# Kernel optimization log

Hardware: AMD Instinct MI355X
Metric: run time of the kernel (lower is better)

## Reference

```python
import jax, jax.numpy as jnp
import numpy as np

DIM = 1024
HEADS = 16
DIM_HEAD = 64
CHUNK = 64
INNER = HEADS * DIM_HEAD  # 1024


def setup_inputs() -> dict:
    key = jax.random.key(0)
    k1, k2, k3 = jax.random.split(key, 3)
    x = jax.random.normal(k1, (4, 4096, DIM), dtype=jnp.float32)
    # nn.Linear weights stored as (out, in); apply as x @ W.T
    w_qkv = jax.random.normal(k2, (INNER * 3, DIM), dtype=jnp.float32) * (DIM ** -0.5)
    w_out = jax.random.normal(k3, (DIM, INNER), dtype=jnp.float32) * (INNER ** -0.5)
    b_out = jnp.zeros((DIM,), dtype=jnp.float32)
    return {"x": x, "w_qkv": w_qkv, "w_out": w_out, "b_out": b_out}


def reference(x, w_qkv, w_out, b_out):
    b, n, _ = x.shape
    scale = DIM_HEAD ** -0.5
    qkv = jnp.einsum('bnd,ed->bne', x, w_qkv)  # (b, n, 3*inner)
    q, k, v = jnp.split(qkv, 3, axis=-1)
    nblk = n // CHUNK

    def to_blocks(t):
        # (b, n, h*d) -> (b, h, nblk, c, d)
        t = t.reshape(b, n, HEADS, DIM_HEAD).transpose(0, 2, 1, 3)
        return t.reshape(b, HEADS, nblk, CHUNK, DIM_HEAD)

    qb, kb, vb = to_blocks(q), to_blocks(k), to_blocks(v)
    scores = jnp.einsum('bhgqd,bhgkd->bhgqk', qb, kb) * scale  # block-local
    attn = jax.nn.softmax(scores, axis=-1)
    ob = jnp.einsum('bhgqk,bhgkd->bhgqd', attn, vb)
    out = ob.reshape(b, HEADS, n, DIM_HEAD).transpose(0, 2, 1, 3).reshape(b, n, INNER)
    return jnp.einsum('bne,de->bnd', out, w_out) + b_out
```

## Files before the change

### kernel.cpp

```cpp
#include <hip/hip_runtime.h>
#include <stdint.h>

typedef __attribute__((ext_vector_type(8))) short bf16x8;
typedef __attribute__((ext_vector_type(4))) float f32x4;

__device__ __forceinline__ unsigned short bf16_of(float f) {
  union { float f; uint32_t u; } x; x.f = f;
  uint32_t r = x.u + 0x7fffu + ((x.u >> 16) & 1u);
  return (unsigned short)(r >> 16);
}

#define GLD16(gp, lp) __builtin_amdgcn_global_load_lds( \
    (const __attribute__((address_space(1))) uint32_t*)(gp), \
    (__attribute__((address_space(3))) uint32_t*)(lp), 16, 0, 0)

#define BAR() do { asm volatile("" ::: "memory"); __builtin_amdgcn_s_barrier(); asm volatile("" ::: "memory"); } while (0)

__global__ void cvt_all(const float* __restrict__ x, const float* __restrict__ wq,
                        const float* __restrict__ wo,
                        unsigned short* __restrict__ xb, unsigned short* __restrict__ wqb,
                        unsigned short* __restrict__ wob) {
  const int N_X = 4194304, N_WQ = 786432, N_WO = 262144;
  const int total = N_X + N_WQ + N_WO;
  int i = blockIdx.x * blockDim.x + threadIdx.x;
  int stride = gridDim.x * blockDim.x;
  for (int j = i; j < total; j += stride) {
    const float* src; unsigned short* dst; int off;
    if (j < N_X)            { src = x;  dst = xb;  off = j; }
    else if (j < N_X + N_WQ){ src = wq; dst = wqb; off = j - N_X; }
    else                    { src = wo; dst = wob; off = j - N_X - N_WQ; }
    float4 f = ((const float4*)src)[off];
    union { unsigned short s[4]; uint2 v; } u;
    u.s[0] = bf16_of(f.x); u.s[1] = bf16_of(f.y);
    u.s[2] = bf16_of(f.z); u.s[3] = bf16_of(f.w);
    ((uint2*)dst)[off] = u.v;
  }
}

template<int BIAS, int OUTF32, int GW, int NSEG>
__global__ __launch_bounds__(512, 2)
void gemm256h(const unsigned short* __restrict__ A,
              const unsigned short* __restrict__ B,
              void* __restrict__ C, const float* __restrict__ bias,
              int N, int K)
{
  __shared__ __align__(1024) unsigned short sm[65536];
  char* const smb = (char*)sm;
  const int tid = threadIdx.x, w = tid >> 6, lane = tid & 63;
  const int wm = w >> 2, wn = w & 3;
  const int fr = lane & 15, kg = lane >> 4;
  const int swz = (fr & 7) << 4;
  const int srow = lane >> 3, sslot = lane & 7;
  const int cXcd = blockIdx.x & 7, iIdx = blockIdx.x >> 3;
  const int NT_tot = NSEG * 16;

  auto tileMN = [&](int s, int& mt, int& nt) {
    const int T = cXcd * (32 * NSEG) + s * 32 + iIdx;
    const int g = T / (64 * GW), rr = T % (64 * GW);
    mt = rr / GW; nt = g * GW + rr % GW;
  };

  int stOff[2][2];
  #pragma unroll
  for (int h = 0; h < 2; ++h)
    #pragma unroll
    for (int i2 = 0; i2 < 2; ++i2)
      stOff[h][i2] = (h * 128 + (i2 * 8 + w) * 8 + srow) * K + (sslot ^ srow) * 8;

  int curMt, curNt, nxtMt, nxtNt;
  tileMN(0, curMt, curNt);
  nxtMt = curMt; nxtNt = curNt;
  if (NSEG > 1) tileMN(1, nxtMt, nxtNt);
  const unsigned short* aSeg  = A + ((size_t)curMt << 8) * K;
  const unsigned short* bSeg  = B + ((size_t)curNt << 8) * K;
  const unsigned short* aSegN = A + ((size_t)nxtMt << 8) * K;
  const unsigned short* bSegN = B + ((size_t)nxtNt << 8) * K;

  auto STAGEh = [&](const unsigned short* src, int opnd, int half, int parity) {
    char* region = smb + opnd * 65536 + parity * 32768 + half * 16384;
    GLD16(src + stOff[half][0], region + w * 1024);
    GLD16(src + stOff[half][1], region + (8 + w) * 1024);
  };
  auto LDA = [&](char* Ab, int j, int kk) -> bf16x8 {
    const int r = 32 * j + 16 * wm + fr;
    return *(const bf16x8*)(Ab + r * 128 + ((kk * 64 + kg * 16) ^ swz));
  };
  auto LDB = [&](char* Bb, int l, int kk) -> bf16x8 {
    const int r = 64 * l + 16 * wn + fr;
    return *(const bf16x8*)(Bb + r * 128 + ((kk * 64 + kg * 16) ^ swz));
  };

  f32x4 acc[8][4] = {};

  STAGEh(bSeg, 1, 0, 0);
  STAGEh(aSeg, 0, 0, 0);
  STAGEh(bSeg, 1, 1, 0);
  STAGEh(aSeg, 0, 1, 0);

  for (int s = 0; s < NSEG; ++s) {
    for (int tt = 0; tt < 16; ++tt) {
      const int T = s * 16 + tt;
      char* Ab = smb + (T & 1) * 32768;
      char* Bb = smb + 65536 + (T & 1) * 32768;

      asm volatile("s_waitcnt vmcnt(0)" ::: "memory");
      BAR();

      bf16x8 a[4][2], bb[4][2];
      #pragma unroll
      for (int l = 0; l < 4; ++l) { bb[l][0] = LDB(Bb, l, 0); bb[l][1] = LDB(Bb, l, 1); }
      #pragma unroll
      for (int j = 0; j < 4; ++j) { a[j][0] = LDA(Ab, j, 0); a[j][1] = LDA(Ab, j, 1); }

      if (T + 1 < NT_tot) {
        const int p1 = (T + 1) & 1;
        const unsigned short *aS, *bS;
        if (tt < 15) { aS = aSeg + ((tt + 1) << 6); bS = bSeg + ((tt + 1) << 6); }
        else         { aS = aSegN;                  bS = bSegN; }
        STAGEh(bS, 1, 0, p1);
        STAGEh(aS, 0, 0, p1);
        STAGEh(bS, 1, 1, p1);
        STAGEh(aS, 0, 1, p1);
      }

      __builtin_amdgcn_s_setprio(1);
      #pragma unroll
      for (int kk = 0; kk < 2; ++kk)
        #pragma unroll
        for (int j = 0; j < 4; ++j)
          #pragma unroll
          for (int l = 0; l < 4; ++l)
            acc[j][l] = __builtin_amdgcn_mfma_f32_16x16x32_bf16(a[j][kk], bb[l][kk], acc[j][l], 0, 0, 0);
      __builtin_amdgcn_s_setprio(0);

      #pragma unroll
      for (int j = 0; j < 4; ++j) { a[j][0] = LDA(Ab, j + 4, 0); a[j][1] = LDA(Ab, j + 4, 1); }
      __builtin_amdgcn_s_setprio(1);
      #pragma unroll
      for (int kk = 0; kk < 2; ++kk)
        #pragma unroll
        for (int j = 0; j < 4; ++j)
          #pragma unroll
          for (int l = 0; l < 4; ++l)
            acc[j + 4][l] = __builtin_amdgcn_mfma_f32_16x16x32_bf16(a[j][kk], bb[l][kk], acc[j + 4][l], 0, 0, 0);
      __builtin_amdgcn_s_setprio(0);
    }

    const int bm0 = curMt << 8, bn0 = curNt << 8;
    #pragma unroll
    for (int l = 0; l < 4; ++l) {
      const int col = bn0 + 64 * l + 16 * wn + fr;
      float bb2 = 0.0f;
      if (BIAS && OUTF32) bb2 = bias[col];
      #pragma unroll
      for (int j = 0; j < 8; ++j) {
        const int row0 = bm0 + 32 * j + 16 * wm + kg * 4;
        #pragma unroll
        for (int rr = 0; rr < 4; ++rr) {
          if (OUTF32)
            ((float*)C)[(size_t)(row0 + rr) * N + col] = acc[j][l][rr] + bb2;
          else
            ((unsigned short*)C)[(size_t)(row0 + rr) * N + col] = bf16_of(acc[j][l][rr]);
        }
      }
    }
    #pragma unroll
    for (int j = 0; j < 8; ++j)
      #pragma unroll
      for (int l = 0; l < 4; ++l)
        acc[j][l] = f32x4{0.f, 0.f, 0.f, 0.f};

    curMt = nxtMt; curNt = nxtNt;
    aSeg = aSegN; bSeg = bSegN;
    if (s + 2 < NSEG) {
      tileMN(s + 2, nxtMt, nxtNt);
      aSegN = A + ((size_t)nxtMt << 8) * K;
      bSegN = B + ((size_t)nxtNt << 8) * K;
    }
  }
}

__global__ __launch_bounds__(256, 4)
void attn_block(const unsigned short* __restrict__ qkv,
                unsigned short* __restrict__ o)
{
  __shared__ __align__(1024) unsigned short Qs[64 * 64];
  __shared__ __align__(1024) unsigned short Ks[64 * 64];
  __shared__ __align__(1024) unsigned short Vt[64 * 64];
  __shared__ __align__(1024) unsigned short Ps[64 * 64];
  __shared__ __align__(1024) unsigned short Os[64 * 64];
  const int tid = threadIdx.x, w = tid >> 6, lane = tid & 63;
  const int g = blockIdx.x, h = blockIdx.y, b = blockIdx.z;
  const size_t mbase = (size_t)b * 4096 + (size_t)g * 64;
  const unsigned short* qg = qkv + mbase * 3072 + h * 64;
  const unsigned short* kgl = qkv + mbase * 3072 + 1024 + h * 64;
  const unsigned short* vg = qkv + mbase * 3072 + 2048 + h * 64;

  #pragma unroll
  for (int i = 0; i < 2; ++i) {
    const int chunk = i * 4 + w;
    const int row = chunk * 8 + (lane >> 3);
    const int c8 = (lane & 7) ^ (row & 7);
    GLD16(qg + (size_t)row * 3072 + c8 * 8, (char*)Qs + chunk * 1024);
    GLD16(kgl + (size_t)row * 3072 + c8 * 8, (char*)Ks + chunk * 1024);
  }
  #pragma unroll
  for (int i = 0; i < 2; ++i) {
    const int c = i * 256 + tid;
    const int n = c >> 3, d0 = (c & 7) * 8;
    bf16x8 v = *(const bf16x8*)(vg + (size_t)n * 3072 + d0);
    #pragma unroll
    for (int j = 0; j < 8; ++j) {
      const int d = d0 + j;
      const int bo = d * 128 + n * 2;
      *(unsigned short*)((char*)Vt + (bo ^ ((d & 7) << 4))) = (unsigned short)v[j];
    }
  }
  __syncthreads();

  const int fr = lane & 15, kg = lane >> 4;
  f32x4 s[4] = {};
  #pragma unroll
  for (int kt = 0; kt < 2; ++kt) {
    const int kb = kt * 64 + kg * 16;
    const int rq = w * 16 + fr;
    bf16x8 aq = *(const bf16x8*)((const char*)Qs + rq * 128 + (kb ^ ((rq & 7) << 4)));
    #pragma unroll
    for (int nf = 0; nf < 4; ++nf) {
      const int rk = nf * 16 + fr;
      bf16x8 bk = *(const bf16x8*)((const char*)Ks + rk * 128 + (kb ^ ((rk & 7) << 4)));
      s[nf] = __builtin_amdgcn_mfma_f32_16x16x32_bf16(aq, bk, s[nf], 0, 0, 0);
    }
  }

  const float scale = 0.125f;
  float inv[4];
  #pragma unroll
  for (int r = 0; r < 4; ++r) {
    float m0 = fmaxf(fmaxf(s[0][r], s[1][r]), fmaxf(s[2][r], s[3][r]));
    #pragma unroll
    for (int d = 1; d < 16; d <<= 1) m0 = fmaxf(m0, __shfl_xor(m0, d));
    float sum = 0.0f;
    #pragma unroll
    for (int nf = 0; nf < 4; ++nf) {
      float p = __expf((s[nf][r] - m0) * scale);
      s[nf][r] = p;
      sum += p;
    }
    #pragma unroll
    for (int d = 1; d < 16; d <<= 1) sum += __shfl_xor(sum, d);
    inv[r] = 1.0f / sum;
  }

  #pragma unroll
  for (int r = 0; r < 4; ++r) {
    const int m = w * 16 + kg * 4 + r;
    #pragma unroll
    for (int nf = 0; nf < 4; ++nf) {
      const int bo = m * 128 + (nf * 16 + fr) * 2;
      *(unsigned short*)((char*)Ps + (bo ^ ((m & 7) << 4))) = bf16_of(s[nf][r] * inv[r]);
    }
  }
  __syncthreads();

  f32x4 oa[4] = {};
  #pragma unroll
  for (int kt = 0; kt < 2; ++kt) {
    const int kb = kt * 64 + kg * 16;
    const int rp = w * 16 + fr;
    bf16x8 ap = *(const bf16x8*)((const char*)Ps + rp * 128 + (kb ^ ((rp & 7) << 4)));
    #pragma unroll
    for (int df = 0; df < 4; ++df) {
      const int rv = df * 16 + fr;
      bf16x8 bv = *(const bf16x8*)((const char*)Vt + rv * 128 + (kb ^ ((rv & 7) << 4)));
      oa[df] = __builtin_amdgcn_mfma_f32_16x16x32_bf16(ap, bv, oa[df], 0, 0, 0);
    }
  }

  #pragma unroll
  for (int df = 0; df < 4; ++df) {
    #pragma unroll
    for (int r = 0; r < 4; ++r) {
      const int m = w * 16 + kg * 4 + r;
      const int bo = m * 128 + (df * 16 + fr) * 2;
      *(unsigned short*)((char*)Os + (bo ^ ((m & 7) << 4))) = bf16_of(oa[df][r]);
    }
  }
  __syncthreads();
  {
    const int row = tid >> 2;
    const int sb = (tid & 3) * 32;
    const int sw = (row & 7) << 4;
    char* rp = (char*)Os + row * 128;
    uint4 v0 = *(uint4*)(rp + (sb ^ sw));
    uint4 v1 = *(uint4*)(rp + ((sb + 16) ^ sw));
    char* op = (char*)(o + (mbase + row) * 1024 + h * 64) + sb;
    *(uint4*)op = v0;
    *(uint4*)(op + 16) = v1;
  }
}

extern "C" void kernel_launch(void* const* d_in, const int* in_sizes, int n_in,
                              void* d_out, int out_size, void* d_ws, size_t ws_size,
                              hipStream_t stream) {
  const float* x     = (const float*)d_in[0];
  const float* w_qkv = (const float*)d_in[1];
  const float* w_out = (const float*)d_in[2];
  const float* b_out = (const float*)d_in[3];
  char* ws = (char*)d_ws;
  const size_t SZ_X  = (size_t)16384 * 1024 * 2;
  const size_t SZ_WQ = (size_t)3072 * 1024 * 2;
  const size_t SZ_WO = (size_t)1024 * 1024 * 2;
  unsigned short* xb  = (unsigned short*)ws;
  unsigned short* wqb = (unsigned short*)(ws + SZ_X);
  unsigned short* wob = (unsigned short*)(ws + SZ_X + SZ_WQ);
  unsigned short* qkv = (unsigned short*)(ws + SZ_X + SZ_WQ + SZ_WO);
  unsigned short* ob  = xb;

  cvt_all<<<2048, 256, 0, stream>>>(x, w_qkv, w_out, xb, wqb, wob);
  gemm256h<0,0,6,3><<<dim3(256), 512, 0, stream>>>(xb, wqb, qkv, nullptr, 3072, 1024);
  attn_block<<<dim3(64, 16, 4), 256, 0, stream>>>(qkv, ob);
  gemm256h<1,1,4,1><<<dim3(256), 512, 0, stream>>>(ob, wob, d_out, b_out, 1024, 1024);
}
```

Measured before the change: 173.5 us.

## Fuse block-local attention with output projection in one kernel

Replaces the separate attention kernel and the output-projection GEMM with one kernel. Each 512-thread workgroup owns 64 rows and loops over all 16 heads: four waves compute attention for the current head, then all eight waves multiply the result by the matching slice of w_out, accumulating into registers. The next head's Q/K/V are double-buffered so their loads overlap the current head's work. This removes the intermediate attention-output round trip through global memory and one launch. In exchange, only 256 single-workgroup blocks run, half the waves sit idle during the attention phase, and w_out is read straight from global memory with no LDS reuse.

```diff
diff --git a/kernel.cpp b/kernel.cpp
--- a/kernel.cpp
+++ b/kernel.cpp
@@ -180,123 +180,163 @@
   }
 }
 
-__global__ __launch_bounds__(256, 4)
-void attn_block(const unsigned short* __restrict__ qkv,
-                unsigned short* __restrict__ o)
+__global__ __launch_bounds__(512, 1)
+void attn_out(const unsigned short* __restrict__ qkv,
+              const unsigned short* __restrict__ wo,
+              const float* __restrict__ bias,
+              float* __restrict__ out)
 {
-  __shared__ __align__(1024) unsigned short Qs[64 * 64];
-  __shared__ __align__(1024) unsigned short Ks[64 * 64];
-  __shared__ __align__(1024) unsigned short Vt[64 * 64];
-  __shared__ __align__(1024) unsigned short Ps[64 * 64];
-  __shared__ __align__(1024) unsigned short Os[64 * 64];
+  __shared__ __align__(1024) unsigned short Qs[2][64 * 64];
+  __shared__ __align__(1024) unsigned short Ks[2][64 * 64];
+  __shared__ __align__(1024) unsigned short Vt[2][64 * 64];
+  __shared__ __align__(1024) unsigned short Pb[64 * 64];
+  __shared__ __align__(1024) unsigned short oaB[64 * 64];
   const int tid = threadIdx.x, w = tid >> 6, lane = tid & 63;
-  const int g = blockIdx.x, h = blockIdx.y, b = blockIdx.z;
-  const size_t mbase = (size_t)b * 4096 + (size_t)g * 64;
-  const unsigned short* qg = qkv + mbase * 3072 + h * 64;
-  const unsigned short* kgl = qkv + mbase * 3072 + 1024 + h * 64;
-  const unsigned short* vg = qkv + mbase * 3072 + 2048 + h * 64;
+  const int fr = lane & 15, kg = lane >> 4;
+  const size_t mb = (size_t)blockIdx.x * 64;
+  const unsigned short* base = qkv + mb * 3072;
+
+  const int srow = w * 8 + (lane >> 3);
+  const int sslot = (lane & 7) ^ (srow & 7);
+  const int vn = tid >> 3, vd0 = (tid & 7) * 8;
+  const float scale = 0.125f;
+
+  f32x4 acc[4][8] = {};
+  bf16x8 vreg;
+
+  GLD16(base + (size_t)srow * 3072 + sslot * 8, (char*)Qs[0] + w * 1024);
+  GLD16(base + (size_t)srow * 3072 + 1024 + sslot * 8, (char*)Ks[0] + w * 1024);
+  vreg = *(const bf16x8*)(base + (size_t)vn * 3072 + 2048 + vd0);
+
+  for (int h = 0; h < 16; ++h) {
+    const int p = h & 1;
+
+    asm volatile("s_waitcnt vmcnt(0)" ::: "memory");
+    #pragma unroll
+    for (int j = 0; j < 8; ++j) {
+      const int d = vd0 + j;
+      const int bo = d * 128 + vn * 2;
+      *(unsigned short*)((char*)Vt[p] + (bo ^ ((d & 7) << 4))) = (unsigned short)vreg[j];
+    }
+    asm volatile("s_waitcnt lgkmcnt(0)" ::: "memory");
+    BAR();
+
+    if (h < 15) {
+      const int q = p ^ 1;
+      const unsigned short* nb = base + (h + 1) * 64;
+      GLD16(nb + (size_t)srow * 3072 + sslot * 8, (char*)Qs[q] + w * 1024);
+      GLD16(nb + (size_t)srow * 3072 + 1024 + sslot * 8, (char*)Ks[q] + w * 1024);
+      vreg = *(const bf16x8*)(nb + (size_t)vn * 3072 + 2048 + vd0);
+    }
+
+    if (w < 4) {
+      f32x4 s[4] = {};
+      #pragma unroll
+      for (int kt = 0; kt < 2; ++kt) {
+        const int kb = kt * 64 + kg * 16;
+        const int rq = w * 16 + fr;
+        bf16x8 aq = *(const bf16x8*)((const char*)Qs[p] + rq * 128 + (kb ^ ((rq & 7) << 4)));
+        #pragma unroll
+        for (int nf = 0; nf < 4; ++nf) {
+          const int rk = nf * 16 + fr;
+          bf16x8 bk = *(const bf16x8*)((const char*)Ks[p] + rk * 128 + (kb ^ ((rk & 7) << 4)));
+          s[nf] = __builtin_amdgcn_mfma_f32_16x16x32_bf16(aq, bk, s[nf], 0, 0, 0);
+        }
+      }
+      float inv[4];
+      #pragma unroll
+      for (int r = 0; r < 4; ++r) {
+        float m0 = fmaxf(fmaxf(s[0][r], s[1][r]), fmaxf(s[2][r], s[3][r]));
+        #pragma unroll
+        for (int d = 1; d < 16; d <<= 1) m0 = fmaxf(m0, __shfl_xor(m0, d));
+        float sum = 0.0f;
+        #pragma unroll
+        for (int nf = 0; nf < 4; ++nf) {
+          float pv = __expf((s[nf][r] - m0) * scale);
+          s[nf][r] = pv;
+          sum += pv;
+        }
+        #pragma unroll
+        for (int d = 1; d < 16; d <<= 1) sum += __shfl_xor(sum, d);
+        inv[r] = 1.0f / sum;
+      }
+      #pragma unroll
+      for (int r = 0; r < 4; ++r) {
+        const int m = w * 16 + kg * 4 + r;
+        #pragma unroll
+        for (int nf = 0; nf < 4; ++nf) {
+          const int bo = m * 128 + (nf * 16 + fr) * 2;
+          *(unsigned short*)((char*)Pb + (bo ^ ((m & 7) << 4))) = bf16_of(s[nf][r] * inv[r]);
+        }
+      }
+      f32x4 oa[4] = {};
+      #pragma unroll
+      for (int kt = 0; kt < 2; ++kt) {
+        const int kb = kt * 64 + kg * 16;
+        const int rp = w * 16 + fr;
+        bf16x8 ap = *(const bf16x8*)((const char*)Pb + rp * 128 + (kb ^ ((rp & 7) << 4)));
+        #pragma unroll
+        for (int df = 0; df < 4; ++df) {
+          const int rv = df * 16 + fr;
+          bf16x8 bv = *(const bf16x8*)((const char*)Vt[p] + rv * 128 + (kb ^ ((rv & 7) << 4)));
+          oa[df] = __builtin_amdgcn_mfma_f32_16x16x32_bf16(ap, bv, oa[df], 0, 0, 0);
+        }
+      }
+      #pragma unroll
+      for (int df = 0; df < 4; ++df) {
+        #pragma unroll
+        for (int r = 0; r < 4; ++r) {
+          const int m = w * 16 + kg * 4 + r;
+          const int bo = m * 128 + (df * 16 + fr) * 2;
+          *(unsigned short*)((char*)oaB + (bo ^ ((m & 7) << 4))) = bf16_of(oa[df][r]);
+        }
+      }
+    }
+
+    bf16x8 bf[8][2];
+    {
+      const unsigned short* ws0 = wo + 64 * h + kg * 8;
+      #pragma unroll
+      for (int nf = 0; nf < 8; ++nf) {
+        const size_t d = (size_t)(128 * w + 16 * nf + fr);
+        bf[nf][0] = *(const bf16x8*)(ws0 + d * 1024);
+        bf[nf][1] = *(const bf16x8*)(ws0 + d * 1024 + 32);
+      }
+    }
+
+    BAR();
+    asm volatile("s_waitcnt vmcnt(0)" ::: "memory");
+
+    bf16x8 afr[4][2];
+    #pragma unroll
+    for (int jm = 0; jm < 4; ++jm) {
+      const int r = 16 * jm + fr;
+      afr[jm][0] = *(const bf16x8*)((const char*)oaB + r * 128 + ((kg * 16) ^ ((r & 7) << 4)));
+      afr[jm][1] = *(const bf16x8*)((const char*)oaB + r * 128 + ((64 + kg * 16) ^ ((r & 7) << 4)));
+    }
+    __builtin_amdgcn_s_setprio(1);
+    #pragma unroll
+    for (int kk = 0; kk < 2; ++kk)
+      #pragma unroll
+      for (int jm = 0; jm < 4; ++jm)
+        #pragma unroll
+        for (int nf = 0; nf < 8; ++nf)
+          acc[jm][nf] = __builtin_amdgcn_mfma_f32_16x16x32_bf16(afr[jm][kk], bf[nf][kk], acc[jm][nf], 0, 0, 0);
+    __builtin_amdgcn_s_setprio(0);
+    BAR();
+  }
 
   #pragma unroll
-  for (int i = 0; i < 2; ++i) {
-    const int chunk = i * 4 + w;
-    const int row = chunk * 8 + (lane >> 3);
-    const int c8 = (lane & 7) ^ (row & 7);
-    GLD16(qg + (size_t)row * 3072 + c8 * 8, (char*)Qs + chunk * 1024);
-    GLD16(kgl + (size_t)row * 3072 + c8 * 8, (char*)Ks + chunk * 1024);
-  }
-  #pragma unroll
-  for (int i = 0; i < 2; ++i) {
-    const int c = i * 256 + tid;
-    const int n = c >> 3, d0 = (c & 7) * 8;
-    bf16x8 v = *(const bf16x8*)(vg + (size_t)n * 3072 + d0);
-    #pragma unroll
-    for (int j = 0; j < 8; ++j) {
-      const int d = d0 + j;
-      const int bo = d * 128 + n * 2;
-      *(unsigned short*)((char*)Vt + (bo ^ ((d & 7) << 4))) = (unsigned short)v[j];
-    }
-  }
-  __syncthreads();
-
-  const int fr = lane & 15, kg = lane >> 4;
-  f32x4 s[4] = {};
-  #pragma unroll
-  for (int kt = 0; kt < 2; ++kt) {
-    const int kb = kt * 64 + kg * 16;
-    const int rq = w * 16 + fr;
-    bf16x8 aq = *(const bf16x8*)((const char*)Qs + rq * 128 + (kb ^ ((rq & 7) << 4)));
-    #pragma unroll
-    for (int nf = 0; nf < 4; ++nf) {
-      const int rk = nf * 16 + fr;
-      bf16x8 bk = *(const bf16x8*)((const char*)Ks + rk * 128 + (kb ^ ((rk & 7) << 4)));
-      s[nf] = __builtin_amdgcn_mfma_f32_16x16x32_bf16(aq, bk, s[nf], 0, 0, 0);
-    }
-  }
-
-  const float scale = 0.125f;
-  float inv[4];
-  #pragma unroll
-  for (int r = 0; r < 4; ++r) {
-    float m0 = fmaxf(fmaxf(s[0][r], s[1][r]), fmaxf(s[2][r], s[3][r]));
-    #pragma unroll
-    for (int d = 1; d < 16; d <<= 1) m0 = fmaxf(m0, __shfl_xor(m0, d));
-    float sum = 0.0f;
-    #pragma unroll
-    for (int nf = 0; nf < 4; ++nf) {
-      float p = __expf((s[nf][r] - m0) * scale);
-      s[nf][r] = p;
-      sum += p;
-    }
-    #pragma unroll
-    for (int d = 1; d < 16; d <<= 1) sum += __shfl_xor(sum, d);
-    inv[r] = 1.0f / sum;
-  }
-
-  #pragma unroll
-  for (int r = 0; r < 4; ++r) {
-    const int m = w * 16 + kg * 4 + r;
-    #pragma unroll
-    for (int nf = 0; nf < 4; ++nf) {
-      const int bo = m * 128 + (nf * 16 + fr) * 2;
-      *(unsigned short*)((char*)Ps + (bo ^ ((m & 7) << 4))) = bf16_of(s[nf][r] * inv[r]);
-    }
-  }
-  __syncthreads();
-
-  f32x4 oa[4] = {};
-  #pragma unroll
-  for (int kt = 0; kt < 2; ++kt) {
-    const int kb = kt * 64 + kg * 16;
-    const int rp = w * 16 + fr;
-    bf16x8 ap = *(const bf16x8*)((const char*)Ps + rp * 128 + (kb ^ ((rp & 7) << 4)));
-    #pragma unroll
-    for (int df = 0; df < 4; ++df) {
-      const int rv = df * 16 + fr;
-      bf16x8 bv = *(const bf16x8*)((const char*)Vt + rv * 128 + (kb ^ ((rv & 7) << 4)));
-      oa[df] = __builtin_amdgcn_mfma_f32_16x16x32_bf16(ap, bv, oa[df], 0, 0, 0);
-    }
-  }
-
-  #pragma unroll
-  for (int df = 0; df < 4; ++df) {
-    #pragma unroll
-    for (int r = 0; r < 4; ++r) {
-      const int m = w * 16 + kg * 4 + r;
-      const int bo = m * 128 + (df * 16 + fr) * 2;
-      *(unsigned short*)((char*)Os + (bo ^ ((m & 7) << 4))) = bf16_of(oa[df][r]);
-    }
-  }
-  __syncthreads();
-  {
-    const int row = tid >> 2;
-    const int sb = (tid & 3) * 32;
-    const int sw = (row & 7) << 4;
-    char* rp = (char*)Os + row * 128;
-    uint4 v0 = *(uint4*)(rp + (sb ^ sw));
-    uint4 v1 = *(uint4*)(rp + ((sb + 16) ^ sw));
-    char* op = (char*)(o + (mbase + row) * 1024 + h * 64) + sb;
-    *(uint4*)op = v0;
-    *(uint4*)(op + 16) = v1;
+  for (int nf = 0; nf < 8; ++nf) {
+    const int d = 128 * w + 16 * nf + fr;
+    const float bb = bias[d];
+    #pragma unroll
+    for (int jm = 0; jm < 4; ++jm) {
+      const size_t row0 = mb + 16 * jm + kg * 4;
+      #pragma unroll
+      for (int rr = 0; rr < 4; ++rr)
+        out[(row0 + rr) * 1024 + d] = acc[jm][nf][rr] + bb;
+    }
   }
 }
 
@@ -315,10 +355,8 @@
   unsigned short* wqb = (unsigned short*)(ws + SZ_X);
   unsigned short* wob = (unsigned short*)(ws + SZ_X + SZ_WQ);
   unsigned short* qkv = (unsigned short*)(ws + SZ_X + SZ_WQ + SZ_WO);
-  unsigned short* ob  = xb;
 
   cvt_all<<<2048, 256, 0, stream>>>(x, w_qkv, w_out, xb, wqb, wob);
   gemm256h<0,0,6,3><<<dim3(256), 512, 0, stream>>>(xb, wqb, qkv, nullptr, 3072, 1024);
-  attn_block<<<dim3(64, 16, 4), 256, 0, stream>>>(qkv, ob);
-  gemm256h<1,1,4,1><<<dim3(256), 512, 0, stream>>>(ob, wob, d_out, b_out, 1024, 1024);
-}
+  attn_out<<<dim3(256), 512, 0, stream>>>(qkv, wob, b_out, (float*)d_out);
+}
```

Result: slower. 255.8 us (+47.5%).
